# Kernel optimization log

Hardware: AMD Instinct MI355X
Metric: run time of the kernel (lower is better)

The kernel has to match this reference:

```python
import math
import jax, jax.numpy as jnp
import numpy as np

N_HEAD = 16

def setup_inputs() -> dict:
    key = jax.random.key(0)
    ks = jax.random.split(key, 3)
    B, T, C = 2, 2048, 1024
    x = jax.random.normal(ks[0], (B, T, C), dtype=jnp.float32)
    W_kqv = jax.random.normal(ks[1], (3 * C, C), dtype=jnp.float32) * 0.02
    b_kqv = jnp.zeros((3 * C,), dtype=jnp.float32)
    W_proj = jax.random.normal(ks[2], (C, C), dtype=jnp.float32) * 0.02
    b_proj = jnp.zeros((C,), dtype=jnp.float32)
    return {"x": x, "W_kqv": W_kqv, "b_kqv": b_kqv, "W_proj": W_proj, "b_proj": b_proj}

def reference(x, W_kqv, b_kqv, W_proj, b_proj):
    B, T, C = x.shape
    nh = N_HEAD
    hd = C // nh
    # fused QKV projection, then view [B,T,nh,3*hd] and slice into k,q,v
    kqv = (x @ W_kqv.T + b_kqv).reshape(B, T, nh, 3, hd)
    k = kqv[..., 0, :]  # [B,T,nh,hd]
    q = kqv[..., 1, :]
    v = kqv[..., 2, :]
    scale = 1.0 / math.sqrt(hd)
    att = jnp.einsum("bthd,bshd->bhts", q, k) * scale  # [B,nh,T,T]
    causal = jnp.tril(jnp.ones((T, T), dtype=bool))
    att = jnp.where(causal[None, None], att, -jnp.inf)
    att = jax.nn.softmax(att, axis=-1)
    y = jnp.einsum("bhts,bshd->bthd", att, v).reshape(B, T, C)
    return y @ W_proj.T + b_proj
```

## Files before the change

kernel.cpp:

```cpp
#include <hip/hip_runtime.h>

#define TSEQ 2048
#define NHEAD 16
#define HD 64
#define CDIM 1024
#define BT 4096

typedef unsigned short u16;
typedef __bf16 bf16x8 __attribute__((ext_vector_type(8)));
typedef float f32x4 __attribute__((ext_vector_type(4)));
typedef float f32x16 __attribute__((ext_vector_type(16)));

union Frag {
  int4 i4;
  bf16x8 b;
  u16 u[8];
};

__device__ __forceinline__ u16 f2b(float f) {
  union { float f; unsigned u; } x;
  x.f = f;
  unsigned r = x.u + 0x7fffu + ((x.u >> 16) & 1u);
  return (u16)(r >> 16);
}

#define N4X 1048576
#define N4W1 786432
#define N4W2 262144
__global__ void cvt3_kernel(const float* __restrict__ x, const float* __restrict__ w1,
                            const float* __restrict__ w2, u16* __restrict__ ox,
                            u16* __restrict__ o1, u16* __restrict__ o2) {
  int i = blockIdx.x * blockDim.x + threadIdx.x;
  int stride = gridDim.x * blockDim.x;
  for (int idx = i; idx < N4X + N4W1 + N4W2; idx += stride) {
    const float4* src;
    ushort4* dst;
    int k;
    if (idx < N4X) { src = (const float4*)x; dst = (ushort4*)ox; k = idx; }
    else if (idx < N4X + N4W1) { src = (const float4*)w1; dst = (ushort4*)o1; k = idx - N4X; }
    else { src = (const float4*)w2; dst = (ushort4*)o2; k = idx - N4X - N4W1; }
    float4 f = src[k];
    ushort4 o;
    o.x = f2b(f.x); o.y = f2b(f.y); o.z = f2b(f.z); o.w = f2b(f.w);
    dst[k] = o;
  }
}

__device__ __forceinline__ void gload_lds16(const u16* g, u16* l) {
  __builtin_amdgcn_global_load_lds((__attribute__((address_space(1))) void*)g,
                                   (__attribute__((address_space(3))) void*)l, 16, 0, 0);
}

__device__ __forceinline__ void gemm_tiles(const u16* __restrict__ A, const u16* __restrict__ Bw,
                                           int K, int m0, int n0,
                                           u16 (*__restrict__ Ash)[128 * 32],
                                           u16 (*__restrict__ Bsh)[128 * 32],
                                           f32x4 acc[4][4]) {
  const int tid = threadIdx.x;
  const int lane = tid & 63;
  const int w = tid >> 6;
  const int wr = (w >> 1) * 64, wc = (w & 1) * 64;
  const int lr = lane & 15;
  const int hi = lane >> 4;
  const int r0 = tid >> 2;
  const int cS = ((tid & 3) ^ ((tid >> 3) & 3)) << 3;
  const int frg = (hi ^ ((lr >> 1) & 3)) << 3;

#define GSTAGE(B, KO)                                                                 \
  { _Pragma("unroll") for (int s = 0; s < 2; s++) {                                   \
      gload_lds16(&A[(size_t)(m0 + s * 64 + r0) * K + (KO) + cS], &Ash[B][(s * 256 + tid) * 8]); \
      gload_lds16(&Bw[(size_t)(n0 + s * 64 + r0) * K + (KO) + cS], &Bsh[B][(s * 256 + tid) * 8]); \
  } }

  GSTAGE(0, 0)
  int cur = 0;
  for (int k0 = 0; k0 < K; k0 += 32) {
    __syncthreads();
    Frag af[4], bfr[4];
#pragma unroll
    for (int i = 0; i < 4; i++) {
      af[i].i4 = *(const int4*)&Ash[cur][(wr + i * 16 + lr) * 32 + frg];
      bfr[i].i4 = *(const int4*)&Bsh[cur][(wc + i * 16 + lr) * 32 + frg];
    }
    __builtin_amdgcn_sched_barrier(0);
    if (k0 + 32 < K) GSTAGE(cur ^ 1, k0 + 32)
    __builtin_amdgcn_sched_barrier(0);
#pragma unroll
    for (int mf = 0; mf < 4; mf++)
#pragma unroll
      for (int nf = 0; nf < 4; nf++)
        acc[mf][nf] = __builtin_amdgcn_mfma_f32_16x16x32_bf16(af[mf].b, bfr[nf].b, acc[mf][nf], 0, 0, 0);
    cur ^= 1;
  }
#undef GSTAGE
}

__global__ __launch_bounds__(256) void gemm_kqv(const u16* __restrict__ xb, const u16* __restrict__ wb,
                                                const float* __restrict__ bias,
                                                u16* __restrict__ qb, u16* __restrict__ kb,
                                                u16* __restrict__ vtb) {
  __shared__ u16 Ash[2][128 * 32];
  __shared__ u16 Bsh[2][128 * 32];
  const int m0 = blockIdx.y * 128, n0 = blockIdx.x * 128;
  f32x4 acc[4][4];
#pragma unroll
  for (int i = 0; i < 4; i++)
#pragma unroll
    for (int j = 0; j < 4; j++) acc[i][j] = (f32x4){0.f, 0.f, 0.f, 0.f};

  gemm_tiles(xb, wb, CDIM, m0, n0, Ash, Bsh, acc);

  const int tid = threadIdx.x;
  const int lane = tid & 63;
  const int w = tid >> 6;
  const int wr = (w >> 1) * 64, wc = (w & 1) * 64;
  const int lr = lane & 15;
  const int rbase = (lane >> 4) << 2;
#pragma unroll
  for (int mf = 0; mf < 4; mf++) {
#pragma unroll
    for (int nf = 0; nf < 4; nf++) {
      f32x4 a = acc[mf][nf];
      int n = n0 + wc + nf * 16 + lr;
      float bval = bias[n];
      int h = n / 192;
      int rem = n - h * 192;
      int s = rem >> 6;
      int d = rem & 63;
      int m00 = m0 + wr + mf * 16 + rbase;
      int bb = m00 >> 11, tt = m00 & 2047;
      int bh = (bb << 4) + h;
      if (s == 2) {
        int t63 = tt & 63;
        int c = (t63 & 51) | ((t63 & 8) >> 1) | ((t63 & 4) << 1);
        ushort4 v4;
        v4.x = f2b(a[0] + bval); v4.y = f2b(a[1] + bval);
        v4.z = f2b(a[2] + bval); v4.w = f2b(a[3] + bval);
        *(ushort4*)&vtb[((size_t)bh * HD + d) * TSEQ + (tt & ~63) + c] = v4;
      } else {
        float scale = (s == 1) ? 0.125f : 1.f;
        u16* dst = (s == 0) ? kb : qb;
#pragma unroll
        for (int r = 0; r < 4; r++)
          dst[((size_t)bh * TSEQ + tt + r) * HD + d] = f2b((a[r] + bval) * scale);
      }
    }
  }
}

__global__ __launch_bounds__(256) void gemm_proj(const u16* __restrict__ yb, const u16* __restrict__ wb,
                                                 const float* __restrict__ bias,
                                                 float* __restrict__ out) {
  __shared__ u16 Ash[2][128 * 32];
  __shared__ u16 Bsh[2][128 * 32];
  const int m0 = blockIdx.y * 128, n0 = blockIdx.x * 128;
  f32x4 acc[4][4];
#pragma unroll
  for (int i = 0; i < 4; i++)
#pragma unroll
    for (int j = 0; j < 4; j++) acc[i][j] = (f32x4){0.f, 0.f, 0.f, 0.f};

  gemm_tiles(yb, wb, CDIM, m0, n0, Ash, Bsh, acc);

  const int tid = threadIdx.x;
  const int lane = tid & 63;
  const int w = tid >> 6;
  const int wr = (w >> 1) * 64, wc = (w & 1) * 64;
  const int lr = lane & 15;
  const int rbase = (lane >> 4) << 2;
#pragma unroll
  for (int mf = 0; mf < 4; mf++) {
#pragma unroll
    for (int nf = 0; nf < 4; nf++) {
      f32x4 a = acc[mf][nf];
      int n = n0 + wc + nf * 16 + lr;
      float bval = bias[n];
#pragma unroll
      for (int r = 0; r < 4; r++) {
        int m = m0 + wr + mf * 16 + rbase + r;
        out[(size_t)m * CDIM + n] = a[r] + bval;
      }
    }
  }
}

__global__ __launch_bounds__(256, 2) void attn_kernel(const u16* __restrict__ qb,
                                                      const u16* __restrict__ kb,
                                                      const u16* __restrict__ vtb,
                                                      u16* __restrict__ yb) {
  __shared__ u16 Ksh[2][64 * 64];
  __shared__ u16 Vsh[2][64 * 64];

  const int tid = threadIdx.x;
  const int lane = tid & 63;
  const int w = tid >> 6;
  const int l31 = lane & 31;
  const int hi32 = lane >> 5;
  const int swz = l31 & 7;

  const int jj = blockIdx.x;
  const int bh = jj & 31;
  const int cls = jj >> 5;
  const int qbk = (cls < 8) ? (15 - cls) : (cls - 8);
  const int q0w = qbk * 128 + w * 32;
  const int LN = 2 * qbk + 2;
  const int jd = q0w >> 6;
  const int qg = q0w + l31;

  const u16* Qp = qb + (size_t)bh * TSEQ * HD;
  const u16* Kp = kb + (size_t)bh * TSEQ * HD;
  const u16* Vt = vtb + (size_t)bh * HD * TSEQ;

  Frag qf[4];
#pragma unroll
  for (int k = 0; k < 4; k++)
    qf[k].i4 = *(const int4*)&Qp[(size_t)(q0w + l31) * HD + k * 16 + hi32 * 8];

  f32x16 O0, O1;
  float lp = 0.f;
#pragma unroll
  for (int i = 0; i < 16; i++) { O0[i] = 0.f; O1[i] = 0.f; }

#define STAGE(B, JT)                                                                 \
  {                                                                                  \
    const int kvb = (JT) * 64;                                                       \
    _Pragma("unroll") for (int p = 0; p < 2; p++) {                                  \
      int c = tid + p * 256;                                                         \
      int row = c >> 3, c16 = c & 7;                                                 \
      int gofs = (c16 ^ (row & 7)) << 3;                                             \
      gload_lds16(&Kp[(size_t)(kvb + row) * HD + gofs], &Ksh[B][c * 8]);             \
      gload_lds16(&Vt[(size_t)row * TSEQ + kvb + gofs], &Vsh[B][c * 8]);             \
    }                                                                                \
  }

#define PACK2(dst, SV, base)                                                         \
    asm("v_cvt_pk_bf16_f32 %0, %1, %2" : "=v"(dst.i4.x) : "v"(SV[base + 0]), "v"(SV[base + 1])); \
    asm("v_cvt_pk_bf16_f32 %0, %1, %2" : "=v"(dst.i4.y) : "v"(SV[base + 2]), "v"(SV[base + 3])); \
    asm("v_cvt_pk_bf16_f32 %0, %1, %2" : "=v"(dst.i4.z) : "v"(SV[base + 4]), "v"(SV[base + 5])); \
    asm("v_cvt_pk_bf16_f32 %0, %1, %2" : "=v"(dst.i4.w) : "v"(SV[base + 6]), "v"(SV[base + 7]));

  STAGE(0, 0)
  int cur = 0;
  for (int jt = 0; jt < LN; ++jt) {
    __syncthreads();
    const int kv0 = jt * 64;
    const bool act = (jt <= jd);
    const bool run1 = (kv0 + 32) <= (q0w + 31);

    Frag ka0[4], ka1[4], vf0[4], vf1[4];
    if (act) {
      const u16* Kt = Ksh[cur];
      const u16* Vl = Vsh[cur];
#pragma unroll
      for (int k = 0; k < 4; k++) {
        int ch = ((2 * k + hi32) ^ swz) << 3;
        ka0[k].i4 = *(const int4*)&Kt[l31 * 64 + ch];
        vf0[k].i4 = *(const int4*)&Vl[l31 * 64 + ch];
        vf1[k].i4 = *(const int4*)&Vl[(32 + l31) * 64 + ch];
      }
      if (run1) {
#pragma unroll
        for (int k = 0; k < 4; k++) {
          int ch = ((2 * k + hi32) ^ swz) << 3;
          ka1[k].i4 = *(const int4*)&Kt[(32 + l31) * 64 + ch];
        }
      }
    }
    __builtin_amdgcn_sched_barrier(0);
    if (jt + 1 < LN) STAGE(cur ^ 1, jt + 1)
    __builtin_amdgcn_sched_barrier(0);
    if (act) {
      const bool diag = (jt == jd);
      f32x16 S;
#pragma unroll
      for (int i = 0; i < 16; i++) S[i] = 0.f;
      __builtin_amdgcn_s_setprio(1);
#pragma unroll
      for (int k = 0; k < 4; k++)
        S = __builtin_amdgcn_mfma_f32_32x32x16_bf16(ka0[k].b, qf[k].b, S, 0, 0, 0);
      __builtin_amdgcn_s_setprio(0);
      if (diag) {
#pragma unroll
        for (int reg = 0; reg < 16; reg++) {
          int crow = (reg & 3) + 8 * (reg >> 2) + 4 * hi32;
          S[reg] = (kv0 + crow <= qg) ? __expf(S[reg]) : 0.f;
        }
      } else {
#pragma unroll
        for (int reg = 0; reg < 16; reg++) S[reg] = __expf(S[reg]);
      }
#pragma unroll
      for (int reg = 0; reg < 16; reg++) lp += S[reg];
      Frag pa[2];
      PACK2(pa[0], S, 0)
      PACK2(pa[1], S, 8)
      __builtin_amdgcn_s_setprio(1);
#pragma unroll
      for (int k = 0; k < 2; k++) {
        O0 = __builtin_amdgcn_mfma_f32_32x32x16_bf16(pa[k].b, vf0[k].b, O0, 0, 0, 0);
        O1 = __builtin_amdgcn_mfma_f32_32x32x16_bf16(pa[k].b, vf1[k].b, O1, 0, 0, 0);
      }
      __builtin_amdgcn_s_setprio(0);
      if (run1) {
        f32x16 T;
#pragma unroll
        for (int i = 0; i < 16; i++) T[i] = 0.f;
        __builtin_amdgcn_s_setprio(1);
#pragma unroll
        for (int k = 0; k < 4; k++)
          T = __builtin_amdgcn_mfma_f32_32x32x16_bf16(ka1[k].b, qf[k].b, T, 0, 0, 0);
        __builtin_amdgcn_s_setprio(0);
        if (diag) {
#pragma unroll
          for (int reg = 0; reg < 16; reg++) {
            int crow = (reg & 3) + 8 * (reg >> 2) + 4 * hi32;
            T[reg] = (kv0 + 32 + crow <= qg) ? __expf(T[reg]) : 0.f;
          }
        } else {
#pragma unroll
          for (int reg = 0; reg < 16; reg++) T[reg] = __expf(T[reg]);
        }
#pragma unroll
        for (int reg = 0; reg < 16; reg++) lp += T[reg];
        Frag pb[2];
        PACK2(pb[0], T, 0)
        PACK2(pb[1], T, 8)
        __builtin_amdgcn_s_setprio(1);
#pragma unroll
        for (int k = 0; k < 2; k++) {
          O0 = __builtin_amdgcn_mfma_f32_32x32x16_bf16(pb[k].b, vf0[k + 2].b, O0, 0, 0, 0);
          O1 = __builtin_amdgcn_mfma_f32_32x32x16_bf16(pb[k].b, vf1[k + 2].b, O1, 0, 0, 0);
        }
        __builtin_amdgcn_s_setprio(0);
      }
    }
    cur ^= 1;
  }
#undef STAGE
#undef PACK2

  float lpt = lp + __shfl_xor(lp, 32);
  const int b = bh >> 4, h = bh & 15;
#pragma unroll
  for (int reg = 0; reg < 16; reg++) {
    int qlocal = (reg & 3) + 8 * (reg >> 2) + 4 * hi32;
    float invr = 1.f / __shfl(lpt, qlocal);
    int t = q0w + qlocal;
    size_t rowoff = ((size_t)(b * TSEQ + t) << 10) + (h << 6);
    yb[rowoff + l31] = f2b(O0[reg] * invr);
    yb[rowoff + 32 + l31] = f2b(O1[reg] * invr);
  }
}

extern "C" void kernel_launch(void* const* d_in, const int* in_sizes, int n_in,
                              void* d_out, int out_size, void* d_ws, size_t ws_size,
                              hipStream_t stream) {
  const float* x = (const float*)d_in[0];
  const float* Wkqv = (const float*)d_in[1];
  const float* bkqv = (const float*)d_in[2];
  const float* Wproj = (const float*)d_in[3];
  const float* bproj = (const float*)d_in[4];
  float* out = (float*)d_out;

  u16* ws = (u16*)d_ws;
  u16* xb = ws;
  u16* wkqvb = xb + 4194304;
  u16* wprojb = wkqvb + 3145728;
  u16* qb = wprojb + 1048576;
  u16* kb = qb + 4194304;
  u16* vtb = kb + 4194304;
  u16* yb = vtb + 4194304;

  cvt3_kernel<<<2048, 256, 0, stream>>>(x, Wkqv, Wproj, xb, wkqvb, wprojb);
  gemm_kqv<<<dim3(24, 32), 256, 0, stream>>>(xb, wkqvb, bkqv, qb, kb, vtb);
  attn_kernel<<<512, 256, 0, stream>>>(qb, kb, vtb, yb);
  gemm_proj<<<dim3(8, 32), 256, 0, stream>>>(yb, wprojb, bproj, out);
}
```

Baseline: 98.07 us.

## Triple-buffer LDS staging in GEMMs and attention, add XCD block swizzle

Switches the GEMM and attention main loops from double to triple buffering, with explicit vmcnt waits so two tiles of global-to-LDS loads stay in flight while the current tile is consumed. It also remaps GEMM workgroup indices so that neighbouring tiles land on the same XCD, to improve L2 reuse. The cost is 1.5x the LDS per block, which could lower occupancy for the attention kernel that targets 2 blocks per CU. The hand-counted vmcnt values must match the number of loads issued per stage.

```diff
diff --git a/kernel.cpp b/kernel.cpp
--- a/kernel.cpp
+++ b/kernel.cpp
@@ -73,35 +73,47 @@
   } }
 
   GSTAGE(0, 0)
-  int cur = 0;
-  for (int k0 = 0; k0 < K; k0 += 32) {
-    __syncthreads();
+  GSTAGE(1, 32)
+  int s0 = 0, s1 = 1, s2 = 2;
+  const int nst = K >> 5;
+  for (int st = 0; st < nst; ++st) {
+    if (st + 1 < nst) asm volatile("s_waitcnt vmcnt(4)" ::: "memory");
+    else              asm volatile("s_waitcnt vmcnt(0)" ::: "memory");
+    __builtin_amdgcn_s_barrier();
     Frag af[4], bfr[4];
+    const u16* Ap = Ash[s0];
+    const u16* Bp = Bsh[s0];
 #pragma unroll
     for (int i = 0; i < 4; i++) {
-      af[i].i4 = *(const int4*)&Ash[cur][(wr + i * 16 + lr) * 32 + frg];
-      bfr[i].i4 = *(const int4*)&Bsh[cur][(wc + i * 16 + lr) * 32 + frg];
+      af[i].i4 = *(const int4*)&Ap[(wr + i * 16 + lr) * 32 + frg];
+      bfr[i].i4 = *(const int4*)&Bp[(wc + i * 16 + lr) * 32 + frg];
     }
     __builtin_amdgcn_sched_barrier(0);
-    if (k0 + 32 < K) GSTAGE(cur ^ 1, k0 + 32)
+    if (st + 2 < nst) GSTAGE(s2, (st + 2) * 32)
     __builtin_amdgcn_sched_barrier(0);
 #pragma unroll
     for (int mf = 0; mf < 4; mf++)
 #pragma unroll
       for (int nf = 0; nf < 4; nf++)
         acc[mf][nf] = __builtin_amdgcn_mfma_f32_16x16x32_bf16(af[mf].b, bfr[nf].b, acc[mf][nf], 0, 0, 0);
-    cur ^= 1;
+    int t_ = s0; s0 = s1; s1 = s2; s2 = t_;
   }
 #undef GSTAGE
+}
+
+__device__ __forceinline__ int xcd_swz(int flat, int nwg) {
+  return (flat & 7) * (nwg >> 3) + (flat >> 3);
 }
 
 __global__ __launch_bounds__(256) void gemm_kqv(const u16* __restrict__ xb, const u16* __restrict__ wb,
                                                 const float* __restrict__ bias,
                                                 u16* __restrict__ qb, u16* __restrict__ kb,
                                                 u16* __restrict__ vtb) {
-  __shared__ u16 Ash[2][128 * 32];
-  __shared__ u16 Bsh[2][128 * 32];
-  const int m0 = blockIdx.y * 128, n0 = blockIdx.x * 128;
+  __shared__ u16 Ash[3][128 * 32];
+  __shared__ u16 Bsh[3][128 * 32];
+  const int nwgx = gridDim.x;
+  const int swz = xcd_swz(blockIdx.y * nwgx + blockIdx.x, nwgx * gridDim.y);
+  const int m0 = (swz / nwgx) * 128, n0 = (swz % nwgx) * 128;
   f32x4 acc[4][4];
 #pragma unroll
   for (int i = 0; i < 4; i++)
@@ -151,9 +163,11 @@
 __global__ __launch_bounds__(256) void gemm_proj(const u16* __restrict__ yb, const u16* __restrict__ wb,
                                                  const float* __restrict__ bias,
                                                  float* __restrict__ out) {
-  __shared__ u16 Ash[2][128 * 32];
-  __shared__ u16 Bsh[2][128 * 32];
-  const int m0 = blockIdx.y * 128, n0 = blockIdx.x * 128;
+  __shared__ u16 Ash[3][128 * 32];
+  __shared__ u16 Bsh[3][128 * 32];
+  const int nwgx = gridDim.x;
+  const int swz = xcd_swz(blockIdx.y * nwgx + blockIdx.x, nwgx * gridDim.y);
+  const int m0 = (swz / nwgx) * 128, n0 = (swz % nwgx) * 128;
   f32x4 acc[4][4];
 #pragma unroll
   for (int i = 0; i < 4; i++)
@@ -188,8 +202,8 @@
                                                       const u16* __restrict__ kb,
                                                       const u16* __restrict__ vtb,
                                                       u16* __restrict__ yb) {
-  __shared__ u16 Ksh[2][64 * 64];
-  __shared__ u16 Vsh[2][64 * 64];
+  __shared__ u16 Ksh[3][64 * 64];
+  __shared__ u16 Vsh[3][64 * 64];
 
   const int tid = threadIdx.x;
   const int lane = tid & 63;
@@ -240,17 +254,20 @@
     asm("v_cvt_pk_bf16_f32 %0, %1, %2" : "=v"(dst.i4.w) : "v"(SV[base + 6]), "v"(SV[base + 7]));
 
   STAGE(0, 0)
-  int cur = 0;
+  STAGE(1, 1)
+  int b0 = 0, b1 = 1, b2 = 2;
   for (int jt = 0; jt < LN; ++jt) {
-    __syncthreads();
+    if (jt + 1 < LN) asm volatile("s_waitcnt vmcnt(4)" ::: "memory");
+    else             asm volatile("s_waitcnt vmcnt(0)" ::: "memory");
+    __builtin_amdgcn_s_barrier();
     const int kv0 = jt * 64;
     const bool act = (jt <= jd);
     const bool run1 = (kv0 + 32) <= (q0w + 31);
 
     Frag ka0[4], ka1[4], vf0[4], vf1[4];
     if (act) {
-      const u16* Kt = Ksh[cur];
-      const u16* Vl = Vsh[cur];
+      const u16* Kt = Ksh[b0];
+      const u16* Vl = Vsh[b0];
 #pragma unroll
       for (int k = 0; k < 4; k++) {
         int ch = ((2 * k + hi32) ^ swz) << 3;
@@ -267,7 +284,7 @@
       }
     }
     __builtin_amdgcn_sched_barrier(0);
-    if (jt + 1 < LN) STAGE(cur ^ 1, jt + 1)
+    if (jt + 2 < LN) STAGE(b2, jt + 2)
     __builtin_amdgcn_sched_barrier(0);
     if (act) {
       const bool diag = (jt == jd);
@@ -334,7 +351,7 @@
         __builtin_amdgcn_s_setprio(0);
       }
     }
-    cur ^= 1;
+    int t_ = b0; b0 = b1; b1 = b2; b2 = t_;
   }
 #undef STAGE
 #undef PACK2
```

New measurement: 107.1 us. 1.09x slower.

## Stage QKV epilogue through LDS for coalesced stores; shrink proj GEMM tile to 64 rows

Applied to the files above, without the earlier changes.

The QKV GEMM epilogue now writes the bias-added, scaled bf16 tile into a swizzled LDS buffer that reuses the staging memory. It then emits 16-byte coalesced stores for Q/K rows and for the permuted transposed V layout, replacing scattered 2-byte global writes. The output projection GEMM switches to 64x128 tiles with a new tile loop, doubling the grid to 512 blocks for better CU occupancy. The cost is an extra LDS round trip and barriers, plus less operand reuse per block in the projection.

```diff
diff --git a/kernel.cpp b/kernel.cpp
--- a/kernel.cpp
+++ b/kernel.cpp
@@ -99,8 +99,9 @@
                                                 const float* __restrict__ bias,
                                                 u16* __restrict__ qb, u16* __restrict__ kb,
                                                 u16* __restrict__ vtb) {
-  __shared__ u16 Ash[2][128 * 32];
-  __shared__ u16 Bsh[2][128 * 32];
+  __shared__ __align__(16) u16 SMEMU[16384];
+  u16 (*Ash)[4096] = (u16(*)[4096])&SMEMU[0];
+  u16 (*Bsh)[4096] = (u16(*)[4096])&SMEMU[8192];
   const int m0 = blockIdx.y * 128, n0 = blockIdx.x * 128;
   f32x4 acc[4][4];
 #pragma unroll
@@ -116,60 +117,140 @@
   const int wr = (w >> 1) * 64, wc = (w & 1) * 64;
   const int lr = lane & 15;
   const int rbase = (lane >> 4) << 2;
+
+  __syncthreads();
+  u16* Csh = SMEMU;
 #pragma unroll
   for (int mf = 0; mf < 4; mf++) {
 #pragma unroll
     for (int nf = 0; nf < 4; nf++) {
       f32x4 a = acc[mf][nf];
-      int n = n0 + wc + nf * 16 + lr;
+      int nl = wc + nf * 16 + lr;
+      int n = n0 + nl;
       float bval = bias[n];
-      int h = n / 192;
-      int rem = n - h * 192;
-      int s = rem >> 6;
-      int d = rem & 63;
-      int m00 = m0 + wr + mf * 16 + rbase;
-      int bb = m00 >> 11, tt = m00 & 2047;
-      int bh = (bb << 4) + h;
-      if (s == 2) {
-        int t63 = tt & 63;
-        int c = (t63 & 51) | ((t63 & 8) >> 1) | ((t63 & 4) << 1);
-        ushort4 v4;
-        v4.x = f2b(a[0] + bval); v4.y = f2b(a[1] + bval);
-        v4.z = f2b(a[2] + bval); v4.w = f2b(a[3] + bval);
-        *(ushort4*)&vtb[((size_t)bh * HD + d) * TSEQ + (tt & ~63) + c] = v4;
-      } else {
-        float scale = (s == 1) ? 0.125f : 1.f;
-        u16* dst = (s == 0) ? kb : qb;
-#pragma unroll
-        for (int r = 0; r < 4; r++)
-          dst[((size_t)bh * TSEQ + tt + r) * HD + d] = f2b((a[r] + bval) * scale);
-      }
-    }
-  }
+      int sres = ((n0 + wc + nf * 16) % 192) >> 6;
+      float scale = (sres == 1) ? 0.125f : 1.f;
+#pragma unroll
+      for (int r = 0; r < 4; r++) {
+        int ml = wr + mf * 16 + rbase + r;
+        Csh[ml * 128 + (nl ^ (((ml >> 2) & 3) << 4))] = f2b((a[r] + bval) * scale);
+      }
+    }
+  }
+  __syncthreads();
+
+  const int bb = m0 >> 11, tt = m0 & 2047;
+#pragma unroll
+  for (int j = 0; j < 2; j++) {
+    int ns = n0 + j * 64;
+    int h = ns / 192;
+    int sres = (ns % 192) >> 6;
+    int bh2 = (bb << 4) + h;
+    if (sres == 2) {
+      int ch = tid & 15;
+      int d0 = tid >> 4;
+#pragma unroll
+      for (int it = 0; it < 4; it++) {
+        int d = d0 + it * 16;
+        unsigned pk[4];
+#pragma unroll
+        for (int p = 0; p < 4; p++) {
+          int c0 = ch * 8 + p * 2;
+          int g0 = c0 >> 6, c6a = c0 & 63;
+          int mA = g0 * 64 + ((c6a & 51) | ((c6a & 8) >> 1) | ((c6a & 4) << 1));
+          int c1 = c0 + 1;
+          int g1 = c1 >> 6, c6b = c1 & 63;
+          int mB = g1 * 64 + ((c6b & 51) | ((c6b & 8) >> 1) | ((c6b & 4) << 1));
+          unsigned lo = Csh[mA * 128 + ((j * 64 + d) ^ (((mA >> 2) & 3) << 4))];
+          unsigned hi2 = Csh[mB * 128 + ((j * 64 + d) ^ (((mB >> 2) & 3) << 4))];
+          pk[p] = lo | (hi2 << 16);
+        }
+        int4 v4; v4.x = pk[0]; v4.y = pk[1]; v4.z = pk[2]; v4.w = pk[3];
+        *(int4*)&vtb[((size_t)bh2 * HD + d) * TSEQ + tt + ch * 8] = v4;
+      }
+    } else {
+      u16* dst = (sres == 0) ? kb : qb;
+      int ch = tid & 7;
+      int rg = tid >> 3;
+#pragma unroll
+      for (int it = 0; it < 4; it++) {
+        int m = rg + it * 32;
+        int ccp = (j * 8 + ch) ^ (((m >> 2) & 3) << 1);
+        int4 v4 = *(const int4*)&Csh[m * 128 + (ccp << 3)];
+        *(int4*)&dst[((size_t)bh2 * TSEQ + tt + m) * HD + ch * 8] = v4;
+      }
+    }
+  }
+}
+
+__device__ __forceinline__ void gemm_tiles64(const u16* __restrict__ A, const u16* __restrict__ Bw,
+                                             int K, int m0, int n0,
+                                             u16 (*__restrict__ Ash)[2048],
+                                             u16 (*__restrict__ Bsh)[4096],
+                                             f32x4 acc[2][4]) {
+  const int tid = threadIdx.x;
+  const int lane = tid & 63;
+  const int w = tid >> 6;
+  const int wr = (w >> 1) * 32, wc = (w & 1) * 64;
+  const int lr = lane & 15;
+  const int hi = lane >> 4;
+  const int r0 = tid >> 2;
+  const int cS = ((tid & 3) ^ ((tid >> 3) & 3)) << 3;
+  const int frg = (hi ^ ((lr >> 1) & 3)) << 3;
+
+#define GSTAGE64(B, KO)                                                               \
+  {                                                                                   \
+    gload_lds16(&A[(size_t)(m0 + r0) * K + (KO) + cS], &Ash[B][tid * 8]);             \
+    _Pragma("unroll") for (int s = 0; s < 2; s++)                                     \
+      gload_lds16(&Bw[(size_t)(n0 + s * 64 + r0) * K + (KO) + cS], &Bsh[B][(s * 256 + tid) * 8]); \
+  }
+
+  GSTAGE64(0, 0)
+  int cur = 0;
+  for (int k0 = 0; k0 < K; k0 += 32) {
+    __syncthreads();
+    Frag af[2], bfr[4];
+#pragma unroll
+    for (int i = 0; i < 2; i++)
+      af[i].i4 = *(const int4*)&Ash[cur][(wr + i * 16 + lr) * 32 + frg];
+#pragma unroll
+    for (int i = 0; i < 4; i++)
+      bfr[i].i4 = *(const int4*)&Bsh[cur][(wc + i * 16 + lr) * 32 + frg];
+    __builtin_amdgcn_sched_barrier(0);
+    if (k0 + 32 < K) GSTAGE64(cur ^ 1, k0 + 32)
+    __builtin_amdgcn_sched_barrier(0);
+#pragma unroll
+    for (int mf = 0; mf < 2; mf++)
+#pragma unroll
+      for (int nf = 0; nf < 4; nf++)
+        acc[mf][nf] = __builtin_amdgcn_mfma_f32_16x16x32_bf16(af[mf].b, bfr[nf].b, acc[mf][nf], 0, 0, 0);
+    cur ^= 1;
+  }
+#undef GSTAGE64
 }
 
 __global__ __launch_bounds__(256) void gemm_proj(const u16* __restrict__ yb, const u16* __restrict__ wb,
                                                  const float* __restrict__ bias,
                                                  float* __restrict__ out) {
-  __shared__ u16 Ash[2][128 * 32];
-  __shared__ u16 Bsh[2][128 * 32];
-  const int m0 = blockIdx.y * 128, n0 = blockIdx.x * 128;
-  f32x4 acc[4][4];
-#pragma unroll
-  for (int i = 0; i < 4; i++)
+  __shared__ __align__(16) u16 Ash[2][2048];
+  __shared__ __align__(16) u16 Bsh[2][4096];
+  const int m0 = blockIdx.y * 64, n0 = blockIdx.x * 128;
+  f32x4 acc[2][4];
+#pragma unroll
+  for (int i = 0; i < 2; i++)
 #pragma unroll
     for (int j = 0; j < 4; j++) acc[i][j] = (f32x4){0.f, 0.f, 0.f, 0.f};
 
-  gemm_tiles(yb, wb, CDIM, m0, n0, Ash, Bsh, acc);
+  gemm_tiles64(yb, wb, CDIM, m0, n0, Ash, Bsh, acc);
 
   const int tid = threadIdx.x;
   const int lane = tid & 63;
   const int w = tid >> 6;
-  const int wr = (w >> 1) * 64, wc = (w & 1) * 64;
+  const int wr = (w >> 1) * 32, wc = (w & 1) * 64;
   const int lr = lane & 15;
   const int rbase = (lane >> 4) << 2;
 #pragma unroll
-  for (int mf = 0; mf < 4; mf++) {
+  for (int mf = 0; mf < 2; mf++) {
 #pragma unroll
     for (int nf = 0; nf < 4; nf++) {
       f32x4 a = acc[mf][nf];
@@ -374,5 +455,5 @@
   cvt3_kernel<<<2048, 256, 0, stream>>>(x, Wkqv, Wproj, xb, wkqvb, wprojb);
   gemm_kqv<<<dim3(24, 32), 256, 0, stream>>>(xb, wkqvb, bkqv, qb, kb, vtb);
   attn_kernel<<<512, 256, 0, stream>>>(qb, kb, vtb, yb);
-  gemm_proj<<<dim3(8, 32), 256, 0, stream>>>(yb, wprojb, bproj, out);
-}
+  gemm_proj<<<dim3(8, 64), 256, 0, stream>>>(yb, wprojb, bproj, out);
+}
```

Measured after the change: 96.00 us. 2.1% less time.
